# Performance work log

Hardware: AMD Instinct MI355X
Metric: run time of the kernel (lower is better)

The kernel has to match this reference:

```python
import jax, jax.numpy as jnp
import numpy as np

LATENT_DIM = 256
NUM_CODEBOOKS = 8
CODEBOOK_SIZE = 512
SUB_DIM = LATENT_DIM // NUM_CODEBOOKS
COMMIT_W = 0.25
CODEBOOK_W = 1.0


def setup_inputs() -> dict:
    key = jax.random.key(0)
    k1, k2 = jax.random.split(key)
    latents = jax.random.normal(k1, (16, 4096, LATENT_DIM), dtype=jnp.float32)
    patch_mask = jnp.ones((16, 4096), dtype=jnp.float32)
    bound = 1.0 / CODEBOOK_SIZE
    codebooks = jax.random.uniform(
        k2, (NUM_CODEBOOKS, CODEBOOK_SIZE, SUB_DIM),
        minval=-bound, maxval=bound, dtype=jnp.float32)
    return {"latents": latents, "patch_mask": patch_mask, "codebooks": codebooks}


def reference(latents, patch_mask, codebooks):
    B, N, D = latents.shape
    C, K, d = codebooks.shape
    x = latents.reshape(B, N, C, d)  # split per codebook

    # squared L2 distances to every codebook entry: (B, N, C, K)
    dist = ((x ** 2).sum(-1, keepdims=True)
            + (codebooks ** 2).sum(-1)[None, None]
            - 2.0 * jnp.einsum('bncd,ckd->bnck', x, codebooks))
    ids = jnp.argmin(dist, axis=-1)  # (B, N, C) int

    # gather nearest entries: (B, N, C, d)
    quant = codebooks[jnp.arange(C)[None, None, :], ids]

    # mse_loss is a mean over equal-sized tensors per codebook, so the mean of
    # per-codebook means equals one global mean
    commitment_loss = jnp.mean((x - jax.lax.stop_gradient(quant)) ** 2) * COMMIT_W
    codebook_loss = jnp.mean((quant - jax.lax.stop_gradient(x)) ** 2) * CODEBOOK_W

    # perplexity over active (masked) patches, per codebook then averaged
    one_hot = jax.nn.one_hot(ids, K, dtype=latents.dtype)  # (B, N, C, K)
    denom = jnp.maximum(patch_mask.sum(), 1.0)
    avg_probs = jnp.einsum('bnck,bn->ck', one_hot, patch_mask) / denom
    perplexity = jnp.mean(jnp.exp(-(avg_probs * jnp.log(avg_probs + 1e-8)).sum(-1)))

    quant_flat = quant.reshape(B, N, D)
    st_quantized = latents + jax.lax.stop_gradient(quant_flat - latents)
    return ids, quant_flat, st_quantized, commitment_loss, codebook_loss, perplexity
```

## Files before the change

### kernel.cpp

```cpp
#include <hip/hip_runtime.h>
#include <math.h>

#define BB 16
#define NN 4096
#define DD 256
#define CC 8
#define KK 512
#define SD 32
#define NTOK (BB * NN)
#define IDS_N (NTOK * CC)
#define QN (NTOK * DD)
#define OFF_Q   (IDS_N)
#define OFF_ST  (IDS_N + QN)
#define OFF_SC  (IDS_N + 2 * QN)

#define GUARD 6e-5f
#define CAP 65536

#define WS_ZERO (32 + 16384)

typedef float f32x4 __attribute__((ext_vector_type(4)));
typedef short s16x8 __attribute__((ext_vector_type(8)));

__device__ __forceinline__ unsigned short f2bf(float f) {
    unsigned u = __float_as_uint(f);
    u += 0x7fffu + ((u >> 16) & 1u);
    return (unsigned short)(u >> 16);
}
__device__ __forceinline__ float bf2f(unsigned short h) {
    return __uint_as_float(((unsigned)h) << 16);
}
__device__ __forceinline__ void split8(const float4 a, const float4 b,
                                       s16x8& hv, s16x8& lv) {
    unsigned short h;
    h = f2bf(a.x); hv[0]=(short)h; lv[0]=(short)f2bf(a.x - bf2f(h));
    h = f2bf(a.y); hv[1]=(short)h; lv[1]=(short)f2bf(a.y - bf2f(h));
    h = f2bf(a.z); hv[2]=(short)h; lv[2]=(short)f2bf(a.z - bf2f(h));
    h = f2bf(a.w); hv[3]=(short)h; lv[3]=(short)f2bf(a.w - bf2f(h));
    h = f2bf(b.x); hv[4]=(short)h; lv[4]=(short)f2bf(b.x - bf2f(h));
    h = f2bf(b.y); hv[5]=(short)h; lv[5]=(short)f2bf(b.y - bf2f(h));
    h = f2bf(b.z); hv[6]=(short)h; lv[6]=(short)f2bf(b.z - bf2f(h));
    h = f2bf(b.w); hv[7]=(short)h; lv[7]=(short)f2bf(b.w - bf2f(h));
}

__global__ __launch_bounds__(256) void vq_prep(
    const float* __restrict__ cbs, const float* __restrict__ mask,
    float* __restrict__ csqf, double* __restrict__ mask_sum)
{
    __shared__ double red[256];
    const int tid = threadIdx.x;
    const int cell = blockIdx.x * 256 + tid;
    const float* cp = cbs + (size_t)cell * SD;
    double s = 0.0;
    #pragma unroll
    for (int j = 0; j < 8; ++j) {
        float4 v = ((const float4*)cp)[j];
        double a = (double)v.x, b = (double)v.y, c = (double)v.z, d = (double)v.w;
        s = fma(a, a, s); s = fma(b, b, s);
        s = fma(c, c, s); s = fma(d, d, s);
    }
    csqf[cell] = (float)s;

    double m = 0.0;
    for (int i = cell; i < NTOK; i += 4096) m += (double)mask[i];
    red[tid] = m;
    __syncthreads();
    for (int st = 128; st > 0; st >>= 1) {
        if (tid < st) red[tid] += red[tid + st];
        __syncthreads();
    }
    if (tid == 0) atomicAdd(mask_sum, red[0]);
}

__global__ __launch_bounds__(512, 4) void vq_score(
    const float* __restrict__ latents, const float* __restrict__ mask,
    const float* __restrict__ cbs, const float* __restrict__ csq_g,
    float* __restrict__ out, double* __restrict__ mse_sum,
    float* __restrict__ hist, unsigned* __restrict__ count,
    unsigned* __restrict__ list)
{
    __shared__ unsigned short s_hi[KK * SD];
    __shared__ unsigned short s_lo[KK * SD];
    __shared__ float  s_csq[KK];
    __shared__ float  s_lhist[KK];
    __shared__ float  s_best[8][32];
    __shared__ float  s_sec[8][32];
    __shared__ int    s_bid[8][32];
    __shared__ double s_mse[8];

    const int tid = threadIdx.x;
    const int c   = blockIdx.x & 7;
    const int tb  = blockIdx.x >> 3;

    {
        const int cw = tid;
        const float* cp = cbs + ((size_t)c * KK + cw) * SD;
        s_csq[cw] = csq_g[c * KK + cw];
        s_lhist[cw] = 0.f;
        #pragma unroll
        for (int q = 0; q < 4; ++q) {
            float4 a = ((const float4*)cp)[2 * q];
            float4 b = ((const float4*)cp)[2 * q + 1];
            s16x8 hv, lv;
            split8(a, b, hv, lv);
            ((s16x8*)(s_hi + (size_t)cw * SD))[q] = hv;
            ((s16x8*)(s_lo + (size_t)cw * SD))[q] = lv;
        }
    }
    __syncthreads();

    const int wv   = tid >> 6;
    const int lane = tid & 63;
    const int col  = lane & 15;
    const int kb   = lane >> 4;

    double mseTot = 0.0;

    #pragma unroll 1
    for (int p = 0; p < 4; ++p) {
        const int tok0 = tb * 1024 + p * 256 + wv * 32;

        s16x8 ah[2], al[2];
        #pragma unroll
        for (int t = 0; t < 2; ++t) {
            const int token = tok0 + t * 16 + col;
            const float4* xp =
                (const float4*)(latents + (size_t)token * DD + c * SD + kb * 8);
            split8(xp[0], xp[1], ah[t], al[t]);
        }

        float best[2][4], sec[2][4]; int bid[2][4];
        #pragma unroll
        for (int t = 0; t < 2; ++t)
            #pragma unroll
            for (int r = 0; r < 4; ++r) {
                best[t][r] = 1e30f; sec[t][r] = 1e30f; bid[t][r] = 0;
            }

        for (int nt = 0; nt < 32; ++nt) {
            const int kcol = nt * 16 + col;
            const float cs = s_csq[kcol];
            const s16x8 bh = *((const s16x8*)(s_hi + (size_t)kcol * SD + kb * 8));
            const s16x8 bl = *((const s16x8*)(s_lo + (size_t)kcol * SD + kb * 8));
            #pragma unroll
            for (int t = 0; t < 2; ++t) {
                f32x4 acc = {0.f, 0.f, 0.f, 0.f};
                acc = __builtin_amdgcn_mfma_f32_16x16x32_bf16(ah[t], bh, acc, 0, 0, 0);
                acc = __builtin_amdgcn_mfma_f32_16x16x32_bf16(ah[t], bl, acc, 0, 0, 0);
                acc = __builtin_amdgcn_mfma_f32_16x16x32_bf16(al[t], bh, acc, 0, 0, 0);
                #pragma unroll
                for (int r = 0; r < 4; ++r) {
                    const float s = fmaf(-2.f, acc[r], cs);
                    const bool lt = s < best[t][r];
                    bid[t][r]  = lt ? kcol : bid[t][r];
                    sec[t][r]  = fminf(sec[t][r], fmaxf(s, best[t][r]));
                    best[t][r] = fminf(best[t][r], s);
                }
            }
        }

        #pragma unroll
        for (int m = 1; m <= 8; m <<= 1) {
            #pragma unroll
            for (int t = 0; t < 2; ++t)
                #pragma unroll
                for (int r = 0; r < 4; ++r) {
                    const float ob = __shfl_xor(best[t][r], m, 64);
                    const float os = __shfl_xor(sec[t][r],  m, 64);
                    const int   oi = __shfl_xor(bid[t][r],  m, 64);
                    const float ns = fminf(fmaxf(best[t][r], ob),
                                           fminf(sec[t][r], os));
                    const bool tk = (ob < best[t][r]) ||
                                    (ob == best[t][r] && oi < bid[t][r]);
                    bid[t][r]  = tk ? oi : bid[t][r];
                    best[t][r] = fminf(best[t][r], ob);
                    sec[t][r]  = ns;
                }
        }

        asm volatile("s_waitcnt lgkmcnt(0)" ::: "memory");
        if (col == 0) {
            #pragma unroll
            for (int t = 0; t < 2; ++t)
                #pragma unroll
                for (int r = 0; r < 4; ++r) {
                    const int idx = t * 16 + kb * 4 + r;
                    s_best[wv][idx] = best[t][r];
                    s_sec[wv][idx]  = sec[t][r];
                    s_bid[wv][idx]  = bid[t][r];
                }
        }
        asm volatile("s_waitcnt lgkmcnt(0)" ::: "memory");

        const int tl    = lane >> 1;
        const int half  = lane & 1;
        const int token = tok0 + tl;
        const float bb  = s_best[wv][tl];
        const float ssv = s_sec[wv][tl];
        const int   bi  = s_bid[wv][tl];
        const bool flag = (ssv - bb) < GUARD;

        const float* qp = cbs + ((size_t)c * KK + bi) * SD + half * 16;
        const float* xp = latents + (size_t)token * DD + c * SD + half * 16;
        float* oq  = out + OFF_Q  + (size_t)token * DD + c * SD + half * 16;
        float* ost = out + OFF_ST + (size_t)token * DD + c * SD + half * 16;
        double acc = 0.0;
        #pragma unroll
        for (int j = 0; j < 4; ++j) {
            float4 qv = ((const float4*)qp)[j];
            float4 xv = ((const float4*)xp)[j];
            float4 sv;
            sv.x = xv.x + (qv.x - xv.x);
            sv.y = xv.y + (qv.y - xv.y);
            sv.z = xv.z + (qv.z - xv.z);
            sv.w = xv.w + (qv.w - xv.w);
            double d;
            d = (double)xv.x - (double)qv.x; acc = fma(d, d, acc);
            d = (double)xv.y - (double)qv.y; acc = fma(d, d, acc);
            d = (double)xv.z - (double)qv.z; acc = fma(d, d, acc);
            d = (double)xv.w - (double)qv.w; acc = fma(d, d, acc);
            ((float4*)oq)[j]  = qv;
            ((float4*)ost)[j] = sv;
        }
        if (!flag) mseTot += acc;
        if (half == 0) {
            out[(size_t)token * CC + c] = (float)bi;
            if (!flag) {
                atomicAdd(&s_lhist[bi], mask[token]);
            } else {
                unsigned slot = atomicAdd(count, 1u);
                if (slot < CAP) list[slot] = ((unsigned)token << 3) | (unsigned)c;
            }
        }
    }

    #pragma unroll
    for (int off = 32; off > 0; off >>= 1)
        mseTot += __shfl_down(mseTot, off, 64);
    if (lane == 0) s_mse[wv] = mseTot;
    __syncthreads();
    if (tid == 0) {
        double s = 0.0;
        #pragma unroll
        for (int w = 0; w < 8; ++w) s += s_mse[w];
        atomicAdd(mse_sum, s);
    }
    {
        float v = s_lhist[tid];
        if (v != 0.f) atomicAdd(&hist[c * KK + tid], v);
    }
}

__global__ __launch_bounds__(256) void vq_resolve(
    const float* __restrict__ latents, const float* __restrict__ mask,
    const float* __restrict__ cbs, const float* __restrict__ csq_g,
    float* __restrict__ out, double* __restrict__ mse_sum,
    float* __restrict__ hist, const unsigned* __restrict__ count,
    const unsigned* __restrict__ list)
{
    unsigned n = *count; if (n > CAP) n = CAP;
    const int lane  = threadIdx.x & 63;
    const int wave  = (blockIdx.x << 2) | (threadIdx.x >> 6);
    const int nwav  = gridDim.x << 2;

    for (unsigned i = wave; i < n; i += nwav) {
        const unsigned e = list[i];
        const int token = (int)(e >> 3), c = (int)(e & 7u);
        const float* xp = latents + (size_t)token * DD + c * SD;

        double xd[SD]; double xs = 0.0;
        #pragma unroll
        for (int j = 0; j < 8; ++j) {
            float4 v = ((const float4*)xp)[j];
            xd[4*j+0] = (double)v.x; xd[4*j+1] = (double)v.y;
            xd[4*j+2] = (double)v.z; xd[4*j+3] = (double)v.w;
            xs = fma((double)v.x, (double)v.x, xs);
            xs = fma((double)v.y, (double)v.y, xs);
            xs = fma((double)v.z, (double)v.z, xs);
            xs = fma((double)v.w, (double)v.w, xs);
        }
        const float xsqf = (float)xs;
        const float* cbase = cbs + (size_t)c * KK * SD;
        const float* csqc  = csq_g + c * KK;

        float best = 1e30f; int bk = lane * 8;
        for (int j = 0; j < 8; ++j) {
            const int k = lane * 8 + j;
            const float* cw = cbase + k * SD;
            double d0 = 0.0, d1 = 0.0, d2 = 0.0, d3 = 0.0;
            #pragma unroll
            for (int q = 0; q < 8; ++q) {
                d0 = fma((double)cw[4*q+0], xd[4*q+0], d0);
                d1 = fma((double)cw[4*q+1], xd[4*q+1], d1);
                d2 = fma((double)cw[4*q+2], xd[4*q+2], d2);
                d3 = fma((double)cw[4*q+3], xd[4*q+3], d3);
            }
            const float dotf = (float)((d0 + d1) + (d2 + d3));
            const float t1 = xsqf + csqc[k];
            const float dist = t1 - 2.0f * dotf;
            if (dist < best) { best = dist; bk = k; }
        }
        #pragma unroll
        for (int off = 32; off > 0; off >>= 1) {
            float od = __shfl_down(best, off, 64);
            int   ok = __shfl_down(bk,   off, 64);
            if (od < best || (od == best && ok < bk)) { best = od; bk = ok; }
        }
        bk = __shfl(bk, 0, 64);

        const int oldid = (int)out[(size_t)token * CC + c];
        if (bk != oldid) {
            if (lane == 0) out[(size_t)token * CC + c] = (float)bk;
            if (lane < SD) {
                float q = cbase[bk * SD + lane];
                float x = xp[lane];
                out[OFF_Q  + (size_t)token * DD + c * SD + lane] = q;
                out[OFF_ST + (size_t)token * DD + c * SD + lane] = x + (q - x);
            }
        }
        double dd = 0.0;
        if (lane < SD) {
            double q = (double)cbase[bk * SD + lane];
            double df = (double)xp[lane] - q;
            dd = df * df;
        }
        #pragma unroll
        for (int off = 32; off > 0; off >>= 1) dd += __shfl_down(dd, off, 64);
        if (lane == 0) {
            atomicAdd(mse_sum, dd);
            atomicAdd(&hist[c * KK + bk], mask[token]);
        }
    }
}

__global__ __launch_bounds__(512) void vq_final(
    const float* __restrict__ hist, const double* __restrict__ mse_sum,
    const double* __restrict__ mask_sum, float* __restrict__ out)
{
    __shared__ double ent[CC];
    const int tid = threadIdx.x;
    double denom = *mask_sum; if (denom < 1.0) denom = 1.0;

    const int w = tid >> 6;
    const int lane = tid & 63;
    double t = 0.0;
    for (int k = lane; k < KK; k += 64) {
        double p = (double)hist[w * KK + k] / denom;
        t += p * log(p + 1e-8);
    }
    #pragma unroll
    for (int off = 32; off > 0; off >>= 1) t += __shfl_down(t, off, 64);
    if (lane == 0) ent[w] = -t;
    __syncthreads();

    if (tid == 0) {
        double mean = mse_sum[0] / (double)QN;
        out[OFF_SC + 0] = (float)(0.25 * mean);
        out[OFF_SC + 1] = (float)(1.0 * mean);
        double perp = 0.0;
        for (int cc = 0; cc < CC; ++cc) perp += exp(ent[cc]);
        out[OFF_SC + 2] = (float)(perp / (double)CC);
    }
}

extern "C" void kernel_launch(void* const* d_in, const int* in_sizes, int n_in,
                              void* d_out, int out_size, void* d_ws, size_t ws_size,
                              hipStream_t stream) {
    const float* latents = (const float*)d_in[0];
    const float* mask    = (const float*)d_in[1];
    const float* cbs     = (const float*)d_in[2];
    float* out = (float*)d_out;

    double*   mse      = (double*)d_ws;
    double*   mask_sum = (double*)((char*)d_ws + 8);
    unsigned* count    = (unsigned*)((char*)d_ws + 16);
    float*    hist     = (float*)((char*)d_ws + 32);
    float*    csqf     = (float*)((char*)d_ws + 32 + 16384);
    unsigned* list     = (unsigned*)((char*)d_ws + 32 + 32768);

    hipMemsetAsync(d_ws, 0, WS_ZERO, stream);

    vq_prep<<<dim3(16), dim3(256), 0, stream>>>(cbs, mask, csqf, mask_sum);
    vq_score<<<dim3(512), dim3(512), 0, stream>>>(
        latents, mask, cbs, csqf, out, mse, hist, count, list);
    vq_resolve<<<dim3(512), dim3(256), 0, stream>>>(
        latents, mask, cbs, csqf, out, mse, hist, count, list);
    vq_final<<<dim3(1), dim3(512), 0, stream>>>(hist, mse, mask_sum, out);
}
```

Baseline: 421.0 us.

## Swizzle codebook LDS layout, use fmed3 for runner-up, retune resolve kernel

The bf16 hi/lo codebook tiles in shared memory are now stored with an XOR swizzle on the 16-byte slot index, so that MFMA operand loads across lanes hit fewer bank conflicts. The second-best distance update becomes a single med3 instruction instead of a min/max pair. The resolve kernel keeps latents as float4 registers rather than a 32-entry double array, unrolls the codeword loop, loads the codebook as float4, gets launch bounds that ask for two blocks per CU, and runs on four times as many blocks. Together these aim to cut LDS conflicts, ALU work and register pressure, though the larger resolve grid only helps if the candidate list is long enough.

```diff
diff --git a/kernel.cpp b/kernel.cpp
--- a/kernel.cpp
+++ b/kernel.cpp
@@ -97,14 +97,15 @@
         const float* cp = cbs + ((size_t)c * KK + cw) * SD;
         s_csq[cw] = csq_g[c * KK + cw];
         s_lhist[cw] = 0.f;
+        const int sw = (cw >> 1) & 3;
         #pragma unroll
         for (int q = 0; q < 4; ++q) {
             float4 a = ((const float4*)cp)[2 * q];
             float4 b = ((const float4*)cp)[2 * q + 1];
             s16x8 hv, lv;
             split8(a, b, hv, lv);
-            ((s16x8*)(s_hi + (size_t)cw * SD))[q] = hv;
-            ((s16x8*)(s_lo + (size_t)cw * SD))[q] = lv;
+            ((s16x8*)(s_hi + (size_t)cw * SD))[q ^ sw] = hv;
+            ((s16x8*)(s_lo + (size_t)cw * SD))[q ^ sw] = lv;
         }
     }
     __syncthreads();
@@ -139,9 +140,10 @@
 
         for (int nt = 0; nt < 32; ++nt) {
             const int kcol = nt * 16 + col;
+            const int slot = kb ^ ((kcol >> 1) & 3);
             const float cs = s_csq[kcol];
-            const s16x8 bh = *((const s16x8*)(s_hi + (size_t)kcol * SD + kb * 8));
-            const s16x8 bl = *((const s16x8*)(s_lo + (size_t)kcol * SD + kb * 8));
+            const s16x8 bh = *((const s16x8*)(s_hi + (size_t)kcol * SD + slot * 8));
+            const s16x8 bl = *((const s16x8*)(s_lo + (size_t)kcol * SD + slot * 8));
             #pragma unroll
             for (int t = 0; t < 2; ++t) {
                 f32x4 acc = {0.f, 0.f, 0.f, 0.f};
@@ -153,7 +155,7 @@
                     const float s = fmaf(-2.f, acc[r], cs);
                     const bool lt = s < best[t][r];
                     bid[t][r]  = lt ? kcol : bid[t][r];
-                    sec[t][r]  = fminf(sec[t][r], fmaxf(s, best[t][r]));
+                    sec[t][r]  = __builtin_amdgcn_fmed3f(s, best[t][r], sec[t][r]);
                     best[t][r] = fminf(best[t][r], s);
                 }
             }
@@ -251,7 +253,7 @@
     }
 }
 
-__global__ __launch_bounds__(256) void vq_resolve(
+__global__ __launch_bounds__(256, 2) void vq_resolve(
     const float* __restrict__ latents, const float* __restrict__ mask,
     const float* __restrict__ cbs, const float* __restrict__ csq_g,
     float* __restrict__ out, double* __restrict__ mse_sum,
@@ -268,32 +270,35 @@
         const int token = (int)(e >> 3), c = (int)(e & 7u);
         const float* xp = latents + (size_t)token * DD + c * SD;
 
-        double xd[SD]; double xs = 0.0;
+        float4 xv[8];
+        #pragma unroll
+        for (int j = 0; j < 8; ++j) xv[j] = ((const float4*)xp)[j];
+
+        double xs = 0.0;
         #pragma unroll
         for (int j = 0; j < 8; ++j) {
-            float4 v = ((const float4*)xp)[j];
-            xd[4*j+0] = (double)v.x; xd[4*j+1] = (double)v.y;
-            xd[4*j+2] = (double)v.z; xd[4*j+3] = (double)v.w;
-            xs = fma((double)v.x, (double)v.x, xs);
-            xs = fma((double)v.y, (double)v.y, xs);
-            xs = fma((double)v.z, (double)v.z, xs);
-            xs = fma((double)v.w, (double)v.w, xs);
+            xs = fma((double)xv[j].x, (double)xv[j].x, xs);
+            xs = fma((double)xv[j].y, (double)xv[j].y, xs);
+            xs = fma((double)xv[j].z, (double)xv[j].z, xs);
+            xs = fma((double)xv[j].w, (double)xv[j].w, xs);
         }
         const float xsqf = (float)xs;
         const float* cbase = cbs + (size_t)c * KK * SD;
         const float* csqc  = csq_g + c * KK;
 
         float best = 1e30f; int bk = lane * 8;
+        #pragma unroll
         for (int j = 0; j < 8; ++j) {
             const int k = lane * 8 + j;
-            const float* cw = cbase + k * SD;
+            const float4* cw = (const float4*)(cbase + k * SD);
             double d0 = 0.0, d1 = 0.0, d2 = 0.0, d3 = 0.0;
             #pragma unroll
             for (int q = 0; q < 8; ++q) {
-                d0 = fma((double)cw[4*q+0], xd[4*q+0], d0);
-                d1 = fma((double)cw[4*q+1], xd[4*q+1], d1);
-                d2 = fma((double)cw[4*q+2], xd[4*q+2], d2);
-                d3 = fma((double)cw[4*q+3], xd[4*q+3], d3);
+                float4 cv = cw[q];
+                d0 = fma((double)cv.x, (double)xv[q].x, d0);
+                d1 = fma((double)cv.y, (double)xv[q].y, d1);
+                d2 = fma((double)cv.z, (double)xv[q].z, d2);
+                d3 = fma((double)cv.w, (double)xv[q].w, d3);
             }
             const float dotf = (float)((d0 + d1) + (d2 + d3));
             const float t1 = xsqf + csqc[k];
@@ -383,7 +388,7 @@
     vq_prep<<<dim3(16), dim3(256), 0, stream>>>(cbs, mask, csqf, mask_sum);
     vq_score<<<dim3(512), dim3(512), 0, stream>>>(
         latents, mask, cbs, csqf, out, mse, hist, count, list);
-    vq_resolve<<<dim3(512), dim3(256), 0, stream>>>(
+    vq_resolve<<<dim3(2048), dim3(256), 0, stream>>>(
         latents, mask, cbs, csqf, out, mse, hist, count, list);
     vq_final<<<dim3(1), dim3(512), 0, stream>>>(hist, mse, mask_sum, out);
 }
```

New measurement: 410.4 us. 2.5% less time.
